# Performance work log

Hardware: AMD Instinct MI355X
Metric: run time of the kernel (lower is better)

## Reference

```python
import jax, jax.numpy as jnp
import numpy as np

B, N, C, M, D, H = 32, 4096, 256, 7, 128, 256
ITERS = 3
EPS = 1e-6       # slot-attention epsilon
LN_EPS = 1e-5    # torch nn.LayerNorm default eps


def _ln(x, w, b):
    m = jnp.mean(x, axis=-1, keepdims=True)
    v = jnp.mean((x - m) ** 2, axis=-1, keepdims=True)
    return (x - m) * jax.lax.rsqrt(v + LN_EPS) * w + b


def setup_inputs() -> dict:
    key = jax.random.key(0)
    ks = jax.random.split(key, 10)
    s = 0.02
    return {
        "inputs": jax.random.normal(ks[0], (B, N, C), jnp.float32),
        "slots_mu": jax.random.normal(ks[1], (B, M, D), jnp.float32),
        "ln_in_w": jnp.ones((C,), jnp.float32), "ln_in_b": jnp.zeros((C,), jnp.float32),
        "ln_slot_w": jnp.ones((D,), jnp.float32), "ln_slot_b": jnp.zeros((D,), jnp.float32),
        "ln_mlp_w": jnp.ones((D,), jnp.float32), "ln_mlp_b": jnp.zeros((D,), jnp.float32),
        "Wq": jax.random.normal(ks[2], (D, D), jnp.float32) * s,
        "Wk": jax.random.normal(ks[3], (D, C), jnp.float32) * s,
        "Wv": jax.random.normal(ks[4], (D, C), jnp.float32) * s,
        "gru_wi": jax.random.normal(ks[5], (3 * D, D), jnp.float32) * s,
        "gru_wh": jax.random.normal(ks[6], (3 * D, D), jnp.float32) * s,
        "gru_bi": jnp.zeros((3 * D,), jnp.float32),
        "gru_bh": jnp.zeros((3 * D,), jnp.float32),
        "mlp_w1": jax.random.normal(ks[7], (H, D), jnp.float32) * s,
        "mlp_b1": jnp.zeros((H,), jnp.float32),
        "mlp_w2": jax.random.normal(ks[8], (D, H), jnp.float32) * s,
        "mlp_b2": jnp.zeros((D,), jnp.float32),
    }


def reference(inputs, slots_mu, ln_in_w, ln_in_b, ln_slot_w, ln_slot_b,
              ln_mlp_w, ln_mlp_b, Wq, Wk, Wv, gru_wi, gru_wh, gru_bi, gru_bh,
              mlp_w1, mlp_b1, mlp_w2, mlp_b2):
    scale = D ** -0.5
    x = _ln(inputs, ln_in_w, ln_in_b)          # [B,N,C]
    k = x @ Wk.T                               # [B,N,D]
    v = x @ Wv.T                               # [B,N,D]
    slots = slots_mu                            # [B,M,D] (used directly, no sampling)
    for _ in range(ITERS):
        slots_prev = slots
        q = _ln(slots, ln_slot_w, ln_slot_b) @ Wq.T              # [B,M,D]
        logits = scale * jnp.einsum('bnd,bmd->bnm', k, q)        # [B,N,M]
        attn = jax.nn.softmax(logits, axis=-1) + EPS             # softmax over slots
        attn = attn / jnp.sum(attn, axis=1, keepdims=True)       # normalize over inputs
        updates = jnp.einsum('bnm,bnd->bmd', attn, v)            # [B,M,D]
        # torch GRUCell: input=updates, hidden=slots_prev
        u = updates.reshape(B * M, D)
        h = slots_prev.reshape(B * M, D)
        gi = u @ gru_wi.T + gru_bi                               # [BM,3D]
        gh = h @ gru_wh.T + gru_bh
        i_r, i_z, i_n = jnp.split(gi, 3, axis=-1)
        h_r, h_z, h_n = jnp.split(gh, 3, axis=-1)
        r = jax.nn.sigmoid(i_r + h_r)
        z = jax.nn.sigmoid(i_z + h_z)
        n = jnp.tanh(i_n + r * h_n)
        slots = ((1.0 - z) * n + z * h).reshape(B, M, D)
        # residual MLP
        y = _ln(slots, ln_mlp_w, ln_mlp_b)
        slots = slots + jax.nn.relu(y @ mlp_w1.T + mlp_b1) @ mlp_w2.T + mlp_b2 * 0 + (jax.nn.relu(y @ mlp_w1.T + mlp_b1) @ mlp_w2.T * 0)
        # (clean form below; keep single expression)
    return slots


# NOTE: the residual line above is intentionally rewritten cleanly here:
def _mlp_residual(slots, ln_mlp_w, ln_mlp_b, mlp_w1, mlp_b1, mlp_w2, mlp_b2):
    y = _ln(slots, ln_mlp_w, ln_mlp_b)
    return slots + (jax.nn.relu(y @ mlp_w1.T + mlp_b1) @ mlp_w2.T + mlp_b2)


def reference(inputs, slots_mu, ln_in_w, ln_in_b, ln_slot_w, ln_slot_b,
              ln_mlp_w, ln_mlp_b, Wq, Wk, Wv, gru_wi, gru_wh, gru_bi, gru_bh,
              mlp_w1, mlp_b1, mlp_w2, mlp_b2):
    scale = D ** -0.5
    x = _ln(inputs, ln_in_w, ln_in_b)          # [B,N,C]
    k = x @ Wk.T                               # [B,N,D]
    v = x @ Wv.T                               # [B,N,D]
    slots = slots_mu                            # [B,M,D]
    for _ in range(ITERS):
        slots_prev = slots
        q = _ln(slots, ln_slot_w, ln_slot_b) @ Wq.T              # [B,M,D]
        logits = scale * jnp.einsum('bnd,bmd->bnm', k, q)        # [B,N,M]
        attn = jax.nn.softmax(logits, axis=-1) + EPS             # softmax over slots
        attn = attn / jnp.sum(attn, axis=1, keepdims=True)       # renormalize over inputs
        updates = jnp.einsum('bnm,bnd->bmd', attn, v)            # [B,M,D]
        u = updates.reshape(B * M, D)
        h = slots_prev.reshape(B * M, D)
        gi = u @ gru_wi.T + gru_bi
        gh = h @ gru_wh.T + gru_bh
        i_r, i_z, i_n = jnp.split(gi, 3, axis=-1)
        h_r, h_z, h_n = jnp.split(gh, 3, axis=-1)
        r = jax.nn.sigmoid(i_r + h_r)
        z = jax.nn.sigmoid(i_z + h_z)
        n = jnp.tanh(i_n + r * h_n)
        slots = ((1.0 - z) * n + z * h).reshape(B, M, D)
        slots = _mlp_residual(slots, ln_mlp_w, ln_mlp_b, mlp_w1, mlp_b1, mlp_w2, mlp_b2)
    return slots
```

## Files before the change

### kernel.cpp

```cpp
#include <hip/hip_runtime.h>
#include <math.h>

#define Bb 32
#define Nn 4096
#define Cc 256
#define Mm 7
#define Dd 128
#define Hh 256
#define ITERS 3
#define EPS 1e-6f
#define LN_EPS 1e-5f
#define SCALE 0.08838834764831845f

typedef __attribute__((ext_vector_type(8))) short bf16x8;
typedef __attribute__((ext_vector_type(4))) float f32x4;

__device__ inline ushort f2bf(float f) {
  uint u = __builtin_bit_cast(uint, f);
  u += 0x7FFF + ((u >> 16) & 1);
  return (ushort)(u >> 16);
}
__device__ inline float bf2f(ushort h) {
  uint u = ((uint)h) << 16;
  return __builtin_bit_cast(float, u);
}
__device__ inline uint pkbf(float a, float b) {
  return (uint)f2bf(a) | ((uint)f2bf(b) << 16);
}

__global__ __launch_bounds__(256) void prep_w2t(
    const float* __restrict__ Wk, const float* __restrict__ Wv,
    const float* __restrict__ lw, const float* __restrict__ lb,
    ushort* __restrict__ Wp, float* __restrict__ Tj, float* __restrict__ Uj) {
  int j = blockIdx.x;
  int c = threadIdx.x;
  float wv = (j < Dd) ? Wk[j * Cc + c] : Wv[(j - Dd) * Cc + c];
  float lwc = lw[c], lbc = lb[c];
  float a = lwc * wv, u = lbc * wv;
  Wp[j * 256 + c] = f2bf(a);
  __shared__ float ra[4], ru[4];
  for (int s = 1; s < 64; s <<= 1) {
    a += __shfl_xor(a, s, 64);
    u += __shfl_xor(u, s, 64);
  }
  int lane = c & 63, w = c >> 6;
  if (lane == 0) { ra[w] = a; ru[w] = u; }
  __syncthreads();
  if (c == 0) {
    Tj[j] = ra[0] + ra[1] + ra[2] + ra[3];
    Uj[j] = ru[0] + ru[1] + ru[2] + ru[3];
  }
}

__global__ __launch_bounds__(256) void prep_trans(
    const float* __restrict__ Wq, const float* __restrict__ wi,
    const float* __restrict__ wh, const float* __restrict__ w1,
    const float* __restrict__ w2, float* __restrict__ WqT,
    float* __restrict__ wiT, float* __restrict__ whT,
    float* __restrict__ w1T, float* __restrict__ w2T) {
  int i = blockIdx.x * 256 + threadIdx.x;
  if (i < 16384) {
    int dd = i >> 7, d = i & 127;
    WqT[i] = Wq[d * 128 + dd];
  } else if (i < 65536) {
    int i2 = i - 16384;
    int dd = i2 / 384, j = i2 % 384;
    wiT[i2] = wi[j * 128 + dd];
  } else if (i < 114688) {
    int i2 = i - 65536;
    int dd = i2 / 384, j = i2 % 384;
    whT[i2] = wh[j * 128 + dd];
  } else if (i < 147456) {
    int i2 = i - 114688;
    int dd = i2 >> 8, j = i2 & 255;
    w1T[i2] = w1[j * 128 + dd];
  } else if (i < 180224) {
    int i2 = i - 147456;
    int j = i2 >> 7, d = i2 & 127;
    w2T[i2] = w2[d * 256 + j];
  }
}

__global__ __launch_bounds__(128) void q_prep0(
    const float* __restrict__ slots_mu, float* __restrict__ slots,
    const float* __restrict__ lsw, const float* __restrict__ lsb,
    const float* __restrict__ WqT, float* __restrict__ qs_g,
    float* __restrict__ num_g, float* __restrict__ den_g) {
  int row = blockIdx.x;
  int t = threadIdx.x;
  __shared__ float ys[128];
  __shared__ float red[4];
  float v = slots_mu[row * 128 + t];
  slots[row * 128 + t] = v;
  float sv = v, sq = v * v;
  for (int s = 1; s < 64; s <<= 1) {
    sv += __shfl_xor(sv, s, 64);
    sq += __shfl_xor(sq, s, 64);
  }
  if ((t & 63) == 0) {
    red[(t >> 6) * 2] = sv;
    red[(t >> 6) * 2 + 1] = sq;
  }
  __syncthreads();
  float tot = red[0] + red[2], totq = red[1] + red[3];
  float mean = tot * (1.f / 128.f);
  float var = totq * (1.f / 128.f) - mean * mean;
  ys[t] = (v - mean) * rsqrtf(var + LN_EPS) * lsw[t] + lsb[t];
  __syncthreads();
  float q = 0.f;
  for (int dd = 0; dd < 128; dd++) q += ys[dd] * WqT[dd * 128 + t];
  qs_g[row * 128 + t] = q;
  num_g[row * 128 + t] = 0.f;
  if (t == 0) den_g[row] = 0.f;
}

__global__ __launch_bounds__(512) void kv_gemm_mfma(
    const float* __restrict__ x, const ushort* __restrict__ Wp,
    const float* __restrict__ Tj, const float* __restrict__ Uj,
    ushort* __restrict__ kg, ushort* __restrict__ vg) {
  __shared__ ushort As[128][40];
  __shared__ ushort Bs[256][40];
  __shared__ float mean_s[128], rstd_s[128];
  int tid = threadIdx.x;
  int lane = tid & 63, w = tid >> 6;
  int wr = w >> 2, wc = w & 3;
  int cl = lane & 15, kq = lane >> 4;
  int row0 = blockIdx.x * 128;

  int ar = tid >> 2;
  int ah = (tid & 3) * 8;
  int bc = tid >> 1;
  int bh = (tid & 1) * 16;
  const float*  xsrc = x  + (size_t)(row0 + ar) * 256 + ah;
  const ushort* wsrc = Wp + (size_t)bc * 256 + bh;

  float s_sum = 0.f, s_sq = 0.f;
  f32x4 acc[4][4] = {};

  for (int k0 = 0; k0 < 256; k0 += 32) {
    float4 xa = *(const float4*)(xsrc + k0);
    float4 xb = *(const float4*)(xsrc + k0 + 4);
    s_sum += xa.x + xa.y + xa.z + xa.w + xb.x + xb.y + xb.z + xb.w;
    s_sq  += xa.x*xa.x + xa.y*xa.y + xa.z*xa.z + xa.w*xa.w
           + xb.x*xb.x + xb.y*xb.y + xb.z*xb.z + xb.w*xb.w;
    uint4 wpack = make_uint4(pkbf(xa.x,xa.y), pkbf(xa.z,xa.w),
                             pkbf(xb.x,xb.y), pkbf(xb.z,xb.w));
    *(uint4*)&As[ar][ah] = wpack;
    *(uint4*)&Bs[bc][bh]     = *(const uint4*)(wsrc + k0);
    *(uint4*)&Bs[bc][bh + 8] = *(const uint4*)(wsrc + k0 + 8);
    __syncthreads();
    bf16x8 af[4], bfr[4];
    #pragma unroll
    for (int i = 0; i < 4; i++) {
      af[i]  = *(const bf16x8*)&As[wr * 64 + i * 16 + cl][kq * 8];
      bfr[i] = *(const bf16x8*)&Bs[wc * 64 + i * 16 + cl][kq * 8];
    }
    #pragma unroll
    for (int mi = 0; mi < 4; mi++)
      #pragma unroll
      for (int ni = 0; ni < 4; ni++)
        acc[mi][ni] = __builtin_amdgcn_mfma_f32_16x16x32_bf16(
            af[mi], bfr[ni], acc[mi][ni], 0, 0, 0);
    __syncthreads();
  }

  s_sum += __shfl_xor(s_sum, 1, 64);
  s_sq  += __shfl_xor(s_sq, 1, 64);
  s_sum += __shfl_xor(s_sum, 2, 64);
  s_sq  += __shfl_xor(s_sq, 2, 64);
  if ((tid & 3) == 0) {
    float mean = s_sum * (1.f / 256.f);
    float var = s_sq * (1.f / 256.f) - mean * mean;
    mean_s[ar] = mean;
    rstd_s[ar] = rsqrtf(var + LN_EPS);
  }
  __syncthreads();

  int rbase = wr * 64 + kq * 4;
  #pragma unroll
  for (int ni = 0; ni < 4; ni++) {
    int c_loc = wc * 64 + ni * 16 + cl;
    float tj = Tj[c_loc];
    float uj = Uj[c_loc];
    ushort* outp = (c_loc < 128) ? kg : vg;
    int cc = c_loc & 127;
    #pragma unroll
    for (int mi = 0; mi < 4; mi++) {
      #pragma unroll
      for (int j = 0; j < 4; j++) {
        int r = rbase + mi * 16 + j;
        float val = rstd_s[r] * (acc[mi][ni][j] - mean_s[r] * tj) + uj;
        outp[(size_t)(row0 + r) * 128 + cc] = f2bf(val);
      }
    }
  }
}

__global__ __launch_bounds__(256) void attn_pass(
    const ushort* __restrict__ kg, const ushort* __restrict__ vg,
    const float* __restrict__ qs_g, float* __restrict__ num_g,
    float* __restrict__ den_g) {
  __shared__ ushort kt[32 * 128];
  __shared__ ushort vt[32 * 128];
  __shared__ float nshare[4 * 896];
  __shared__ float dshare[28];
  int tid = threadIdx.x;
  int lane = tid & 63, w = tid >> 6;
  int g = lane >> 4, s16 = lane & 15;
  int b = blockIdx.y;
  int cb = blockIdx.x;

  float qrf[7][8];
  #pragma unroll
  for (int m = 0; m < 7; m++) {
    float4 qa = *(const float4*)&qs_g[b * 896 + m * 128 + s16 * 8];
    float4 qb = *(const float4*)&qs_g[b * 896 + m * 128 + s16 * 8 + 4];
    qrf[m][0]=qa.x; qrf[m][1]=qa.y; qrf[m][2]=qa.z; qrf[m][3]=qa.w;
    qrf[m][4]=qb.x; qrf[m][5]=qb.y; qrf[m][6]=qb.z; qrf[m][7]=qb.w;
  }
  float numr[7][8] = {};
  float denr[7] = {};
  const ushort* kb = kg + ((size_t)b * Nn + cb * 128) * 128;
  const ushort* vb = vg + ((size_t)b * Nn + cb * 128) * 128;

  for (int t = 0; t < 4; t++) {
    for (int i = tid; i < 512; i += 256) {
      int r = i >> 4;
      int c8 = (i & 15) * 8;
      *(uint4*)&kt[r * 128 + c8] = *(const uint4*)&kb[(size_t)(t * 32 + r) * 128 + c8];
      *(uint4*)&vt[r * 128 + c8] = *(const uint4*)&vb[(size_t)(t * 32 + r) * 128 + c8];
    }
    __syncthreads();
    #pragma unroll
    for (int batch = 0; batch < 2; batch++) {
      int r = w * 8 + batch * 4 + g;
      uint4 kk = *(uint4*)&kt[r * 128 + s16 * 8];
      float kf[8];
      kf[0]=bf2f((ushort)(kk.x&0xffff)); kf[1]=bf2f((ushort)(kk.x>>16));
      kf[2]=bf2f((ushort)(kk.y&0xffff)); kf[3]=bf2f((ushort)(kk.y>>16));
      kf[4]=bf2f((ushort)(kk.z&0xffff)); kf[5]=bf2f((ushort)(kk.z>>16));
      kf[6]=bf2f((ushort)(kk.w&0xffff)); kf[7]=bf2f((ushort)(kk.w>>16));
      float p[7];
      #pragma unroll
      for (int m = 0; m < 7; m++) {
        float a = 0.f;
        #pragma unroll
        for (int j = 0; j < 8; j++) a += kf[j] * qrf[m][j];
        p[m] = a;
      }
      #pragma unroll
      for (int s = 1; s < 16; s <<= 1)
        #pragma unroll
        for (int m = 0; m < 7; m++) p[m] += __shfl_xor(p[m], s, 64);
      float mx = -1e30f;
      #pragma unroll
      for (int m = 0; m < 7; m++) { p[m] *= SCALE; mx = fmaxf(mx, p[m]); }
      float se = 0.f, e[7];
      #pragma unroll
      for (int m = 0; m < 7; m++) { e[m] = __expf(p[m] - mx); se += e[m]; }
      float inv = 1.f / se;
      uint4 vv = *(uint4*)&vt[r * 128 + s16 * 8];
      float vf[8];
      vf[0]=bf2f((ushort)(vv.x&0xffff)); vf[1]=bf2f((ushort)(vv.x>>16));
      vf[2]=bf2f((ushort)(vv.y&0xffff)); vf[3]=bf2f((ushort)(vv.y>>16));
      vf[4]=bf2f((ushort)(vv.z&0xffff)); vf[5]=bf2f((ushort)(vv.z>>16));
      vf[6]=bf2f((ushort)(vv.w&0xffff)); vf[7]=bf2f((ushort)(vv.w>>16));
      #pragma unroll
      for (int m = 0; m < 7; m++) {
        float a = e[m] * inv + EPS;
        denr[m] += a;
        #pragma unroll
        for (int j = 0; j < 8; j++) numr[m][j] += a * vf[j];
      }
    }
    __syncthreads();
  }

  #pragma unroll
  for (int m = 0; m < 7; m++) {
    #pragma unroll
    for (int j = 0; j < 8; j++) {
      numr[m][j] += __shfl_xor(numr[m][j], 16, 64);
      numr[m][j] += __shfl_xor(numr[m][j], 32, 64);
    }
    denr[m] += __shfl_xor(denr[m], 16, 64);
    denr[m] += __shfl_xor(denr[m], 32, 64);
  }
  if (g == 0) {
    #pragma unroll
    for (int m = 0; m < 7; m++) {
      float4 n0 = make_float4(numr[m][0], numr[m][1], numr[m][2], numr[m][3]);
      float4 n1 = make_float4(numr[m][4], numr[m][5], numr[m][6], numr[m][7]);
      *(float4*)&nshare[w * 896 + m * 128 + s16 * 8]     = n0;
      *(float4*)&nshare[w * 896 + m * 128 + s16 * 8 + 4] = n1;
    }
  }
  if (lane == 0) {
    #pragma unroll
    for (int m = 0; m < 7; m++) dshare[w * 7 + m] = denr[m];
  }
  __syncthreads();
  for (int i = tid; i < 896; i += 256) {
    float s = nshare[i] + nshare[896 + i] + nshare[1792 + i] + nshare[2688 + i];
    atomicAdd(&num_g[b * 896 + i], s);
  }
  if (tid < 7) {
    float s = dshare[tid] + dshare[7 + tid] + dshare[14 + tid] + dshare[21 + tid];
    atomicAdd(&den_g[b * 7 + tid], s);
  }
}

__global__ __launch_bounds__(128) void gru_mlp(
    float* __restrict__ num_g, float* __restrict__ den_g,
    float* __restrict__ slots, const float* __restrict__ wiT,
    const float* __restrict__ whT, const float* __restrict__ gbi,
    const float* __restrict__ gbh, const float* __restrict__ w1T,
    const float* __restrict__ w2T, const float* __restrict__ b1,
    const float* __restrict__ b2, const float* __restrict__ lmw,
    const float* __restrict__ lmb, const float* __restrict__ lsw,
    const float* __restrict__ lsb, const float* __restrict__ WqT,
    float* __restrict__ qs_g) {
  int row = blockIdx.x;
  int t = threadIdx.x;
  __shared__ float us[128], hs[128], ys[128], hid[256];
  __shared__ float red[4];
  float den = den_g[row];
  float u = num_g[row * 128 + t] / den;
  float h = slots[row * 128 + t];
  us[t] = u;
  hs[t] = h;
  __syncthreads();
  float gr = gbi[t], gz = gbi[128 + t], gn = gbi[256 + t];
  float hr = gbh[t], hz = gbh[128 + t], hn = gbh[256 + t];
  for (int dd = 0; dd < 128; dd++) {
    float uv = us[dd], hv = hs[dd];
    const float* wi = wiT + dd * 384;
    const float* wh = whT + dd * 384;
    gr += uv * wi[t];
    gz += uv * wi[128 + t];
    gn += uv * wi[256 + t];
    hr += hv * wh[t];
    hz += hv * wh[128 + t];
    hn += hv * wh[256 + t];
  }
  float r = 1.f / (1.f + __expf(-(gr + hr)));
  float z = 1.f / (1.f + __expf(-(gz + hz)));
  float n = tanhf(gn + r * hn);
  float sn = (1.f - z) * n + z * h;
  float sv = sn, sq = sn * sn;
  for (int s = 1; s < 64; s <<= 1) {
    sv += __shfl_xor(sv, s, 64);
    sq += __shfl_xor(sq, s, 64);
  }
  if ((t & 63) == 0) {
    red[(t >> 6) * 2] = sv;
    red[(t >> 6) * 2 + 1] = sq;
  }
  __syncthreads();
  float tot = red[0] + red[2], totq = red[1] + red[3];
  float mean = tot * (1.f / 128.f);
  float var = totq * (1.f / 128.f) - mean * mean;
  float y = (sn - mean) * rsqrtf(var + LN_EPS) * lmw[t] + lmb[t];
  ys[t] = y;
  __syncthreads();
  float h0 = b1[t], h1 = b1[128 + t];
  for (int dd = 0; dd < 128; dd++) {
    float yv = ys[dd];
    h0 += yv * w1T[dd * 256 + t];
    h1 += yv * w1T[dd * 256 + 128 + t];
  }
  hid[t] = fmaxf(h0, 0.f);
  hid[128 + t] = fmaxf(h1, 0.f);
  __syncthreads();
  float o = sn + b2[t];
  for (int j = 0; j < 256; j++) o += hid[j] * w2T[j * 128 + t];
  slots[row * 128 + t] = o;
  float sv2 = o, sq2 = o * o;
  for (int s = 1; s < 64; s <<= 1) {
    sv2 += __shfl_xor(sv2, s, 64);
    sq2 += __shfl_xor(sq2, s, 64);
  }
  if ((t & 63) == 0) {
    red[(t >> 6) * 2] = sv2;
    red[(t >> 6) * 2 + 1] = sq2;
  }
  __syncthreads();
  float tot2 = red[0] + red[2], totq2 = red[1] + red[3];
  float mean2 = tot2 * (1.f / 128.f);
  float var2 = totq2 * (1.f / 128.f) - mean2 * mean2;
  float y2 = (o - mean2) * rsqrtf(var2 + LN_EPS) * lsw[t] + lsb[t];
  ys[t] = y2;
  __syncthreads();
  float q = 0.f;
  for (int dd = 0; dd < 128; dd++) q += ys[dd] * WqT[dd * 128 + t];
  qs_g[row * 128 + t] = q;
  num_g[row * 128 + t] = 0.f;
  if (t == 0) den_g[row] = 0.f;
}

extern "C" void kernel_launch(void* const* d_in, const int* in_sizes, int n_in,
                              void* d_out, int out_size, void* d_ws, size_t ws_size,
                              hipStream_t stream) {
  (void)in_sizes; (void)n_in; (void)out_size; (void)ws_size;
  const float* inputs  = (const float*)d_in[0];
  const float* slots_mu= (const float*)d_in[1];
  const float* ln_in_w = (const float*)d_in[2];
  const float* ln_in_b = (const float*)d_in[3];
  const float* ln_sl_w = (const float*)d_in[4];
  const float* ln_sl_b = (const float*)d_in[5];
  const float* ln_ml_w = (const float*)d_in[6];
  const float* ln_ml_b = (const float*)d_in[7];
  const float* Wq      = (const float*)d_in[8];
  const float* Wk      = (const float*)d_in[9];
  const float* Wv      = (const float*)d_in[10];
  const float* gru_wi  = (const float*)d_in[11];
  const float* gru_wh  = (const float*)d_in[12];
  const float* gru_bi  = (const float*)d_in[13];
  const float* gru_bh  = (const float*)d_in[14];
  const float* mlp_w1  = (const float*)d_in[15];
  const float* mlp_b1  = (const float*)d_in[16];
  const float* mlp_w2  = (const float*)d_in[17];
  const float* mlp_b2  = (const float*)d_in[18];
  float* slots = (float*)d_out;

  char* base = (char*)d_ws;
  size_t o = 0;
  ushort* kg = (ushort*)(base + o); o += (size_t)Bb * Nn * Dd * 2;
  ushort* vg = (ushort*)(base + o); o += (size_t)Bb * Nn * Dd * 2;
  ushort* Wp = (ushort*)(base + o); o += 256 * 256 * 2;
  float* Tj  = (float*)(base + o); o += 256 * 4;
  float* Uj  = (float*)(base + o); o += 256 * 4;
  float* WqT = (float*)(base + o); o += 128 * 128 * 4;
  float* wiT = (float*)(base + o); o += 384 * 128 * 4;
  float* whT = (float*)(base + o); o += 384 * 128 * 4;
  float* w1T = (float*)(base + o); o += 256 * 128 * 4;
  float* w2T = (float*)(base + o); o += 256 * 128 * 4;
  float* num_g = (float*)(base + o); o += (size_t)Bb * Mm * Dd * 4;
  float* den_g = (float*)(base + o); o += (size_t)Bb * Mm * 4;
  float* qs_g  = (float*)(base + o); o += (size_t)Bb * Mm * Dd * 4;

  prep_w2t<<<256, 256, 0, stream>>>(Wk, Wv, ln_in_w, ln_in_b, Wp, Tj, Uj);
  prep_trans<<<704, 256, 0, stream>>>(Wq, gru_wi, gru_wh, mlp_w1, mlp_w2,
                                      WqT, wiT, whT, w1T, w2T);
  q_prep0<<<Bb * Mm, 128, 0, stream>>>(slots_mu, slots, ln_sl_w, ln_sl_b,
                                       WqT, qs_g, num_g, den_g);
  kv_gemm_mfma<<<(Bb * Nn) / 128, 512, 0, stream>>>(inputs, Wp, Tj, Uj, kg, vg);
  for (int it = 0; it < ITERS; it++) {
    attn_pass<<<dim3(Nn / 128, Bb), 256, 0, stream>>>(kg, vg, qs_g, num_g, den_g);
    gru_mlp<<<Bb * Mm, 128, 0, stream>>>(num_g, den_g, slots, wiT, whT,
                                         gru_bi, gru_bh, w1T, w2T,
                                         mlp_b1, mlp_b2, ln_ml_w, ln_ml_b,
                                         ln_sl_w, ln_sl_b, WqT, qs_g);
  }
}
```

Before: 448.2 us.

## Register-prefetch K/V in attention pass and fold softmax scale into Wq

The attention pass drops its shared-memory staging and barriers. Each wave now loads its own 32 rows of K and V straight from global memory into registers, double-buffered, so the next row's load is issued before the current row is computed. The softmax scale and log2(e) are folded into the transposed Wq, which lets the kernel call exp2 directly and skip the max subtraction and the scale multiply. The projection GEMM also prefetches the next k-tile into registers before the barrier. Dropping the max subtraction risks overflow if logits grow large, and the extra prefetch registers raise register pressure.

Result: faster. 433.7 us (-3.3%).

```diff
diff --git a/kernel.cpp b/kernel.cpp
--- a/kernel.cpp
+++ b/kernel.cpp
@@ -10,7 +10,7 @@
 #define ITERS 3
 #define EPS 1e-6f
 #define LN_EPS 1e-5f
-#define SCALE 0.08838834764831845f
+#define QSCALE 0.12751743f
 
 typedef __attribute__((ext_vector_type(8))) short bf16x8;
 typedef __attribute__((ext_vector_type(4))) float f32x4;
@@ -26,6 +26,12 @@
 }
 __device__ inline uint pkbf(float a, float b) {
   return (uint)f2bf(a) | ((uint)f2bf(b) << 16);
+}
+__device__ inline float bflo(uint u) {
+  return __builtin_bit_cast(float, u << 16);
+}
+__device__ inline float bfhi(uint u) {
+  return __builtin_bit_cast(float, u & 0xffff0000u);
 }
 
 __global__ __launch_bounds__(256) void prep_w2t(
@@ -61,7 +67,7 @@
   int i = blockIdx.x * 256 + threadIdx.x;
   if (i < 16384) {
     int dd = i >> 7, d = i & 127;
-    WqT[i] = Wq[d * 128 + dd];
+    WqT[i] = Wq[d * 128 + dd] * QSCALE;
   } else if (i < 65536) {
     int i2 = i - 16384;
     int dd = i2 / 384, j = i2 % 384;
@@ -137,17 +143,26 @@
   float s_sum = 0.f, s_sq = 0.f;
   f32x4 acc[4][4] = {};
 
+  float4 xa = *(const float4*)(xsrc);
+  float4 xb = *(const float4*)(xsrc + 4);
+  uint4 wb0 = *(const uint4*)(wsrc);
+  uint4 wb1 = *(const uint4*)(wsrc + 8);
+
   for (int k0 = 0; k0 < 256; k0 += 32) {
-    float4 xa = *(const float4*)(xsrc + k0);
-    float4 xb = *(const float4*)(xsrc + k0 + 4);
     s_sum += xa.x + xa.y + xa.z + xa.w + xb.x + xb.y + xb.z + xb.w;
     s_sq  += xa.x*xa.x + xa.y*xa.y + xa.z*xa.z + xa.w*xa.w
            + xb.x*xb.x + xb.y*xb.y + xb.z*xb.z + xb.w*xb.w;
     uint4 wpack = make_uint4(pkbf(xa.x,xa.y), pkbf(xa.z,xa.w),
                              pkbf(xb.x,xb.y), pkbf(xb.z,xb.w));
     *(uint4*)&As[ar][ah] = wpack;
-    *(uint4*)&Bs[bc][bh]     = *(const uint4*)(wsrc + k0);
-    *(uint4*)&Bs[bc][bh + 8] = *(const uint4*)(wsrc + k0 + 8);
+    *(uint4*)&Bs[bc][bh]     = wb0;
+    *(uint4*)&Bs[bc][bh + 8] = wb1;
+    if (k0 < 224) {
+      xa  = *(const float4*)(xsrc + k0 + 32);
+      xb  = *(const float4*)(xsrc + k0 + 36);
+      wb0 = *(const uint4*)(wsrc + k0 + 32);
+      wb1 = *(const uint4*)(wsrc + k0 + 40);
+    }
     __syncthreads();
     bf16x8 af[4], bfr[4];
     #pragma unroll
@@ -200,8 +215,6 @@
     const ushort* __restrict__ kg, const ushort* __restrict__ vg,
     const float* __restrict__ qs_g, float* __restrict__ num_g,
     float* __restrict__ den_g) {
-  __shared__ ushort kt[32 * 128];
-  __shared__ ushort vt[32 * 128];
   __shared__ float nshare[4 * 896];
   __shared__ float dshare[28];
   int tid = threadIdx.x;
@@ -220,60 +233,54 @@
   }
   float numr[7][8] = {};
   float denr[7] = {};
-  const ushort* kb = kg + ((size_t)b * Nn + cb * 128) * 128;
-  const ushort* vb = vg + ((size_t)b * Nn + cb * 128) * 128;
-
-  for (int t = 0; t < 4; t++) {
-    for (int i = tid; i < 512; i += 256) {
-      int r = i >> 4;
-      int c8 = (i & 15) * 8;
-      *(uint4*)&kt[r * 128 + c8] = *(const uint4*)&kb[(size_t)(t * 32 + r) * 128 + c8];
-      *(uint4*)&vt[r * 128 + c8] = *(const uint4*)&vb[(size_t)(t * 32 + r) * 128 + c8];
-    }
-    __syncthreads();
-    #pragma unroll
-    for (int batch = 0; batch < 2; batch++) {
-      int r = w * 8 + batch * 4 + g;
-      uint4 kk = *(uint4*)&kt[r * 128 + s16 * 8];
-      float kf[8];
-      kf[0]=bf2f((ushort)(kk.x&0xffff)); kf[1]=bf2f((ushort)(kk.x>>16));
-      kf[2]=bf2f((ushort)(kk.y&0xffff)); kf[3]=bf2f((ushort)(kk.y>>16));
-      kf[4]=bf2f((ushort)(kk.z&0xffff)); kf[5]=bf2f((ushort)(kk.z>>16));
-      kf[6]=bf2f((ushort)(kk.w&0xffff)); kf[7]=bf2f((ushort)(kk.w>>16));
-      float p[7];
+
+  size_t base = ((size_t)b * Nn + (size_t)cb * 128 + w * 32) * 128;
+  const ushort* kp = kg + base;
+  const ushort* vp = vg + base;
+  int loff = g * 128 + s16 * 8;
+
+  uint4 kb0 = *(const uint4*)&kp[loff];
+  uint4 vb0 = *(const uint4*)&vp[loff];
+  uint4 kb1, vb1;
+
+  #pragma unroll
+  for (int it = 0; it < 8; it++) {
+    uint4 kk = (it & 1) ? kb1 : kb0;
+    uint4 vv = (it & 1) ? vb1 : vb0;
+    if (it < 7) {
+      int noff = (it + 1) * 512 + loff;
+      if (it & 1) { kb0 = *(const uint4*)&kp[noff]; vb0 = *(const uint4*)&vp[noff]; }
+      else        { kb1 = *(const uint4*)&kp[noff]; vb1 = *(const uint4*)&vp[noff]; }
+    }
+    float kf[8];
+    kf[0]=bflo(kk.x); kf[1]=bfhi(kk.x); kf[2]=bflo(kk.y); kf[3]=bfhi(kk.y);
+    kf[4]=bflo(kk.z); kf[5]=bfhi(kk.z); kf[6]=bflo(kk.w); kf[7]=bfhi(kk.w);
+    float p[7];
+    #pragma unroll
+    for (int m = 0; m < 7; m++) {
+      float a = 0.f;
       #pragma unroll
-      for (int m = 0; m < 7; m++) {
-        float a = 0.f;
-        #pragma unroll
-        for (int j = 0; j < 8; j++) a += kf[j] * qrf[m][j];
-        p[m] = a;
-      }
+      for (int j = 0; j < 8; j++) a += kf[j] * qrf[m][j];
+      p[m] = a;
+    }
+    #pragma unroll
+    for (int s = 1; s < 16; s <<= 1)
       #pragma unroll
-      for (int s = 1; s < 16; s <<= 1)
-        #pragma unroll
-        for (int m = 0; m < 7; m++) p[m] += __shfl_xor(p[m], s, 64);
-      float mx = -1e30f;
+      for (int m = 0; m < 7; m++) p[m] += __shfl_xor(p[m], s, 64);
+    float e[7], se = 0.f;
+    #pragma unroll
+    for (int m = 0; m < 7; m++) { e[m] = exp2f(p[m]); se += e[m]; }
+    float inv = __builtin_amdgcn_rcpf(se);
+    float vf[8];
+    vf[0]=bflo(vv.x); vf[1]=bfhi(vv.x); vf[2]=bflo(vv.y); vf[3]=bfhi(vv.y);
+    vf[4]=bflo(vv.z); vf[5]=bfhi(vv.z); vf[6]=bflo(vv.w); vf[7]=bfhi(vv.w);
+    #pragma unroll
+    for (int m = 0; m < 7; m++) {
+      float a = e[m] * inv + EPS;
+      denr[m] += a;
       #pragma unroll
-      for (int m = 0; m < 7; m++) { p[m] *= SCALE; mx = fmaxf(mx, p[m]); }
-      float se = 0.f, e[7];
-      #pragma unroll
-      for (int m = 0; m < 7; m++) { e[m] = __expf(p[m] - mx); se += e[m]; }
-      float inv = 1.f / se;
-      uint4 vv = *(uint4*)&vt[r * 128 + s16 * 8];
-      float vf[8];
-      vf[0]=bf2f((ushort)(vv.x&0xffff)); vf[1]=bf2f((ushort)(vv.x>>16));
-      vf[2]=bf2f((ushort)(vv.y&0xffff)); vf[3]=bf2f((ushort)(vv.y>>16));
-      vf[4]=bf2f((ushort)(vv.z&0xffff)); vf[5]=bf2f((ushort)(vv.z>>16));
-      vf[6]=bf2f((ushort)(vv.w&0xffff)); vf[7]=bf2f((ushort)(vv.w>>16));
-      #pragma unroll
-      for (int m = 0; m < 7; m++) {
-        float a = e[m] * inv + EPS;
-        denr[m] += a;
-        #pragma unroll
-        for (int j = 0; j < 8; j++) numr[m][j] += a * vf[j];
-      }
-    }
-    __syncthreads();
+      for (int j = 0; j < 8; j++) numr[m][j] += a * vf[j];
+    }
   }
 
   #pragma unroll
```
